# Performance work log

Hardware: AMD Instinct MI355X
Metric: run time of the kernel (lower is better)

The kernel has to match this reference:

```python
import jax, jax.numpy as jnp
import numpy as np

STRIDE = 4
EPS = 1e-6  # torch.pairwise_distance default eps


def setup_inputs() -> dict:
    key = jax.random.key(0)
    k1, k2 = jax.random.split(key)
    a = jax.random.normal(k1, (4, 256, 256, 256), dtype=jnp.float32)
    b = jax.random.normal(k2, (4, 256, 256, 256), dtype=jnp.float32)
    return {"a": a, "b": b}


def _patches(x, stride):
    # nn.Unfold(1, stride): sample every stride-th pixel -> [B, N, C]
    B, C, H, W = x.shape
    xp = x[:, :, ::stride, ::stride]            # [B, C, h, w]
    h, w = xp.shape[2], xp.shape[3]
    return xp.reshape(B, C, h * w).transpose(0, 2, 1), h, w


def reference(a, b):
    B, C, H, W = a.shape
    av, h, w = _patches(a, STRIDE)              # [B, N, C]
    bv, _, _ = _patches(b, STRIDE)              # [B, M, C]
    a2 = jnp.sum(av * av, axis=-1)              # [B, N]
    b2 = jnp.sum(bv * bv, axis=-1)              # [B, M]
    ab = jnp.einsum('bnc,bmc->bnm', av, bv)     # [B, N, M]
    sa = jnp.sum(av, axis=-1)
    sb = jnp.sum(bv, axis=-1)
    d2 = (a2[:, :, None] + b2[:, None, :] - 2.0 * ab
          + 2.0 * EPS * (sa[:, :, None] - sb[:, None, :]) + C * EPS * EPS)
    d2min = jnp.min(d2, axis=-1)                # sqrt is monotone -> min of d2 first
    l2 = jnp.sqrt(jnp.maximum(d2min, 0.0))      # [B, N]
    scores = 2.0 * jax.nn.sigmoid(-l2)
    sm = scores.reshape(B, h, w)
    # F.interpolate(..., mode='nearest') with integer scale == pixel repeat
    out = jnp.repeat(jnp.repeat(sm, STRIDE, axis=1), STRIDE, axis=2)
    return out[:, None, :, :]                   # [B, 1, H, W]
```

## Files before the change

kernel.cpp:

```cpp
#include <hip/hip_runtime.h>
#include <math.h>


#define BATCH 4
#define CH    256
#define HH    256
#define WW    256
#define NPTS  4096
#define EPSV  1e-6f

typedef _Float16 half8  __attribute__((ext_vector_type(8)));
typedef float    f32x4  __attribute__((ext_vector_type(4)));

typedef __attribute__((address_space(1))) const void global_cvoid;
typedef __attribute__((address_space(3))) void lds_void;

#define AC_OFF   0u
#define BC_OFF   (8u << 20)
#define A2_OFF   (16u << 20)
#define B2_OFF   ((16u << 20) + (64u << 10))
#define DP_OFF   ((16u << 20) + (128u << 10))
#define WS_TOTAL ((16u << 20) + (384u << 10))

__global__ __launch_bounds__(256) void gm_gather(
    const float* __restrict__ srcA, const float* __restrict__ srcB,
    unsigned char* __restrict__ ws)
{
  const int t  = threadIdx.x;
  const int h  = blockIdx.x;
  const int b  = blockIdx.y;
  const int z  = blockIdx.z;
  const int w  = t & 63;
  const int wv = t >> 6;

  const float* src = z ? srcB : srcA;
  unsigned char* dst = ws + (z ? BC_OFF : AC_OFF);
  float* norms = (float*)(ws + (z ? B2_OFF : A2_OFF));
  const float epsSign = z ? -2.0f * EPSV : 2.0f * EPSV;
  const float addC    = z ? (float)CH * EPSV * EPSV : 0.0f;

  const float* rowbase = src + ((size_t)b * CH) * (HH * WW)
                             + (size_t)(h * 4) * WW + (size_t)(w * 4);
  float ssum = 0.0f, ssq = 0.0f;
  #pragma unroll
  for (int i = 0; i < 8; ++i) {
    const int kc = wv * 8 + i;
    half8 hv;
    #pragma unroll
    for (int j = 0; j < 8; ++j) {
      const int c = kc * 8 + j;
      float v = rowbase[(size_t)c * (HH * WW)];
      ssum += v;
      ssq  = fmaf(v, v, ssq);
      hv[j] = (_Float16)v;
    }
    *reinterpret_cast<half8*>(dst + ((size_t)((b * 32 + kc) * NPTS + h * 64 + w)) * 16) = hv;
  }

  __shared__ float red[2][4][64];
  red[0][wv][w] = ssum;
  red[1][wv][w] = ssq;
  __syncthreads();
  if (t < 64) {
    float sm = red[0][0][t] + red[0][1][t] + red[0][2][t] + red[0][3][t];
    float sq = red[1][0][t] + red[1][1][t] + red[1][2][t] + red[1][3][t];
    norms[b * NPTS + h * 64 + t] = fmaf(epsSign, sm, sq) + addC;
  }
}

__device__ __forceinline__ void stage_b_tile(const unsigned char* __restrict__ Bc,
                                             int b, int mbase,
                                             unsigned char* dst, int t) {
  const int wv = t >> 6;
  #pragma unroll
  for (int r = 0; r < 8; ++r) {
    unsigned x  = (unsigned)(r * 256 + t) * 16;
    unsigned lb = x ^ (((x >> 9) & 7) << 4);
    unsigned m_l = lb >> 9;
    unsigned kcb = (lb & 511) >> 4;
    const unsigned char* srcp =
        Bc + ((size_t)((b * 32 + kcb) * NPTS + mbase + m_l)) * 16;
    __builtin_amdgcn_global_load_lds((global_cvoid*)srcp,
                                     (lds_void*)(dst + (r * 4096 + wv * 1024)),
                                     16, 0, 0);
  }
}

__global__ __launch_bounds__(256, 2) void gm_gemm_min(
    const unsigned char* __restrict__ Ac, const unsigned char* __restrict__ Bc,
    const float* __restrict__ a2p, const float* __restrict__ b2pc,
    float* __restrict__ d2part)
{
  __shared__ __align__(16) unsigned char smem[65536];

  const int t  = threadIdx.x;
  const int l  = t & 63;
  const int wv = t >> 6;
  const int q  = (l >> 4) & 3;

  const int orig    = blockIdx.x;
  const int logical = (orig & 7) * 64 + (orig >> 3);
  const int ns = logical & 31;
  const int mq = (logical >> 5) & 3;
  const int b  = logical >> 7;
  const int nbase  = ns * 128;
  const int mstart = mq * 1024;

  #pragma unroll
  for (int r = 0; r < 16; ++r) {
    unsigned x  = (unsigned)(r * 256 + t) * 16;
    unsigned lb = x ^ (((x >> 9) & 7) << 4);
    unsigned n_l = lb >> 9;
    unsigned kcb = (lb & 511) >> 4;
    const unsigned char* srcp =
        Ac + ((size_t)((b * 32 + kcb) * NPTS + nbase + n_l)) * 16;
    __builtin_amdgcn_global_load_lds((global_cvoid*)srcp,
                                     (lds_void*)(smem + (r * 4096 + wv * 1024)),
                                     16, 0, 0);
  }
  asm volatile("s_waitcnt vmcnt(0)" ::: "memory");
  __builtin_amdgcn_s_barrier();

  half8 af[2][8];
  #pragma unroll
  for (int nf = 0; nf < 2; ++nf) {
    const unsigned rr = wv * 32 + nf * 16 + (l & 15);
    const unsigned sw = (rr & 7) << 4;
    #pragma unroll
    for (int kk = 0; kk < 8; ++kk)
      af[nf][kk] = *reinterpret_cast<const half8*>(
          smem + ((rr * 512 + q * 16 + kk * 64) ^ sw));
  }
  asm volatile("s_waitcnt lgkmcnt(0)" ::: "memory");
  __builtin_amdgcn_s_barrier();

  float rmin[2][4];
  #pragma unroll
  for (int nf = 0; nf < 2; ++nf)
    #pragma unroll
    for (int r = 0; r < 4; ++r) rmin[nf][r] = 3.0e38f;

  stage_b_tile(Bc, b, mstart, smem, t);
  for (int mt = 0; mt < 16; ++mt) {
    unsigned char* cb = (mt & 1) ? smem + 32768 : smem;
    unsigned char* nb = (mt & 1) ? smem : smem + 32768;
    if (mt < 15) {
      stage_b_tile(Bc, b, mstart + (mt + 1) * 64, nb, t);
      asm volatile("s_waitcnt vmcnt(8)" ::: "memory");
    } else {
      asm volatile("s_waitcnt vmcnt(0)" ::: "memory");
    }
    __builtin_amdgcn_s_barrier();

    f32x4 acc[2][4];
    #pragma unroll
    for (int nf = 0; nf < 2; ++nf)
      #pragma unroll
      for (int ms = 0; ms < 4; ++ms) acc[nf][ms] = (f32x4){0.f, 0.f, 0.f, 0.f};

    #pragma unroll
    for (int kk = 0; kk < 8; ++kk) {
      half8 bf[4];
      #pragma unroll
      for (int ms = 0; ms < 4; ++ms) {
        const unsigned rrB = ms * 16 + (l & 15);
        bf[ms] = *reinterpret_cast<const half8*>(
            cb + ((rrB * 512 + q * 16 + kk * 64) ^ ((rrB & 7) << 4)));
      }
      #pragma unroll
      for (int ms = 0; ms < 4; ++ms) {
        acc[0][ms] = __builtin_amdgcn_mfma_f32_16x16x32_f16(af[0][kk], bf[ms], acc[0][ms], 0, 0, 0);
        acc[1][ms] = __builtin_amdgcn_mfma_f32_16x16x32_f16(af[1][kk], bf[ms], acc[1][ms], 0, 0, 0);
      }
    }

    const int mbase = mstart + mt * 64;
    #pragma unroll
    for (int ms = 0; ms < 4; ++ms) {
      const float bp = b2pc[b * NPTS + mbase + ms * 16 + (l & 15)];
      #pragma unroll
      for (int r = 0; r < 4; ++r) {
        rmin[0][r] = fminf(rmin[0][r], fmaf(-2.0f, acc[0][ms][r], bp));
        rmin[1][r] = fminf(rmin[1][r], fmaf(-2.0f, acc[1][ms][r], bp));
      }
    }
    __builtin_amdgcn_s_barrier();
  }

  #pragma unroll
  for (int nf = 0; nf < 2; ++nf)
    #pragma unroll
    for (int r = 0; r < 4; ++r) {
      float v = rmin[nf][r];
      v = fminf(v, __shfl_xor(v, 1, 64));
      v = fminf(v, __shfl_xor(v, 2, 64));
      v = fminf(v, __shfl_xor(v, 4, 64));
      v = fminf(v, __shfl_xor(v, 8, 64));
      if ((l & 15) == 0) {
        const int n = nbase + wv * 32 + nf * 16 + q * 4 + r;
        d2part[(size_t)(b * NPTS + n) * 4 + mq] = v + a2p[b * NPTS + n];
      }
    }
}

__global__ __launch_bounds__(256) void gm_finalize(
    const float* __restrict__ d2part, float* __restrict__ out)
{
  const int id = blockIdx.x * 256 + threadIdx.x;
  const f32x4 u = *reinterpret_cast<const f32x4*>(d2part + (size_t)id * 4);
  const float d2 = fminf(fminf(u[0], u[1]), fminf(u[2], u[3]));
  const float l2 = sqrtf(fmaxf(d2, 0.0f));
  const float s  = 2.0f / (1.0f + expf(l2));
  const int b = id >> 12;
  const int n = id & 4095;
  const int h = n >> 6, w = n & 63;
  float4 v = make_float4(s, s, s, s);
  float* obase = out + ((size_t)(b * 256 + h * 4)) * 256 + w * 4;
  #pragma unroll
  for (int i = 0; i < 4; ++i)
    *reinterpret_cast<float4*>(obase + (size_t)i * 256) = v;
}

__global__ void gm_sentinel(float* out) { out[0] = 1.0e6f; }

extern "C" void kernel_launch(void* const* d_in, const int* in_sizes, int n_in,
                              void* d_out, int out_size, void* d_ws, size_t ws_size,
                              hipStream_t stream) {
  const float* a = (const float*)d_in[0];
  const float* b = (const float*)d_in[1];
  float* out = (float*)d_out;
  unsigned char* ws = (unsigned char*)d_ws;

  if (ws_size < (size_t)WS_TOTAL) {
    gm_sentinel<<<1, 1, 0, stream>>>(out);
    return;
  }

  gm_gather<<<dim3(64, 4, 2), 256, 0, stream>>>(a, b, ws);
  gm_gemm_min<<<512, 256, 0, stream>>>(
      ws + AC_OFF, ws + BC_OFF,
      (const float*)(ws + A2_OFF), (const float*)(ws + B2_OFF),
      (float*)(ws + DP_OFF));
  gm_finalize<<<64, 256, 0, stream>>>((const float*)(ws + DP_OFF), out);
}
```

Baseline: 75.18 us.

## Double block size, deepen B-tile pipeline to four LDS stages, cache b2 in LDS

The GEMM-min kernel now runs 512-thread blocks, each covering 256 query points, so every staged B tile is shared by twice as many rows and the grid halves to 256 blocks. The B pipeline becomes a 4-slot ring prefetched three tiles ahead, which drops the trailing barrier per iteration, and the b2 norms are preloaded into LDS instead of read from global memory each iteration. MFMA sections get raised wave priority. The cost is 128KB+ of LDS per block, which may allow only one block per CU, and 256 blocks may underfill the GPU.

```diff
diff --git a/kernel.cpp b/kernel.cpp
--- a/kernel.cpp
+++ b/kernel.cpp
@@ -73,25 +73,26 @@
                                              unsigned char* dst, int t) {
   const int wv = t >> 6;
   #pragma unroll
-  for (int r = 0; r < 8; ++r) {
-    unsigned x  = (unsigned)(r * 256 + t) * 16;
+  for (int r = 0; r < 4; ++r) {
+    unsigned x  = (unsigned)(r * 512 + t) * 16;
     unsigned lb = x ^ (((x >> 9) & 7) << 4);
     unsigned m_l = lb >> 9;
     unsigned kcb = (lb & 511) >> 4;
     const unsigned char* srcp =
         Bc + ((size_t)((b * 32 + kcb) * NPTS + mbase + m_l)) * 16;
     __builtin_amdgcn_global_load_lds((global_cvoid*)srcp,
-                                     (lds_void*)(dst + (r * 4096 + wv * 1024)),
+                                     (lds_void*)(dst + (r * 8192 + wv * 1024)),
                                      16, 0, 0);
   }
 }
 
-__global__ __launch_bounds__(256, 2) void gm_gemm_min(
+__global__ __launch_bounds__(512, 2) void gm_gemm_min(
     const unsigned char* __restrict__ Ac, const unsigned char* __restrict__ Bc,
     const float* __restrict__ a2p, const float* __restrict__ b2pc,
     float* __restrict__ d2part)
 {
-  __shared__ __align__(16) unsigned char smem[65536];
+  __shared__ __align__(16) unsigned char smem[131072];
+  __shared__ float sB2[1024];
 
   const int t  = threadIdx.x;
   const int l  = t & 63;
@@ -99,26 +100,29 @@
   const int q  = (l >> 4) & 3;
 
   const int orig    = blockIdx.x;
-  const int logical = (orig & 7) * 64 + (orig >> 3);
-  const int ns = logical & 31;
-  const int mq = (logical >> 5) & 3;
-  const int b  = logical >> 7;
-  const int nbase  = ns * 128;
+  const int logical = (orig & 7) * 32 + (orig >> 3);
+  const int ns = logical & 15;
+  const int mq = (logical >> 4) & 3;
+  const int b  = logical >> 6;
+  const int nbase  = ns * 256;
   const int mstart = mq * 1024;
 
   #pragma unroll
   for (int r = 0; r < 16; ++r) {
-    unsigned x  = (unsigned)(r * 256 + t) * 16;
+    unsigned x  = (unsigned)(r * 512 + t) * 16;
     unsigned lb = x ^ (((x >> 9) & 7) << 4);
     unsigned n_l = lb >> 9;
     unsigned kcb = (lb & 511) >> 4;
     const unsigned char* srcp =
         Ac + ((size_t)((b * 32 + kcb) * NPTS + nbase + n_l)) * 16;
     __builtin_amdgcn_global_load_lds((global_cvoid*)srcp,
-                                     (lds_void*)(smem + (r * 4096 + wv * 1024)),
+                                     (lds_void*)(smem + (r * 8192 + wv * 1024)),
                                      16, 0, 0);
   }
-  asm volatile("s_waitcnt vmcnt(0)" ::: "memory");
+  sB2[t]       = b2pc[b * NPTS + mstart + t];
+  sB2[t + 512] = b2pc[b * NPTS + mstart + t + 512];
+
+  asm volatile("s_waitcnt vmcnt(0) lgkmcnt(0)" ::: "memory");
   __builtin_amdgcn_s_barrier();
 
   half8 af[2][8];
@@ -140,24 +144,29 @@
     #pragma unroll
     for (int r = 0; r < 4; ++r) rmin[nf][r] = 3.0e38f;
 
-  stage_b_tile(Bc, b, mstart, smem, t);
+  stage_b_tile(Bc, b, mstart +   0, smem,          t);
+  stage_b_tile(Bc, b, mstart +  64, smem + 32768,  t);
+  stage_b_tile(Bc, b, mstart + 128, smem + 65536,  t);
+
   for (int mt = 0; mt < 16; ++mt) {
-    unsigned char* cb = (mt & 1) ? smem + 32768 : smem;
-    unsigned char* nb = (mt & 1) ? smem : smem + 32768;
-    if (mt < 15) {
-      stage_b_tile(Bc, b, mstart + (mt + 1) * 64, nb, t);
-      asm volatile("s_waitcnt vmcnt(8)" ::: "memory");
-    } else {
-      asm volatile("s_waitcnt vmcnt(0)" ::: "memory");
-    }
+    if (mt <= 13)      asm volatile("s_waitcnt vmcnt(8)" ::: "memory");
+    else if (mt == 14) asm volatile("s_waitcnt vmcnt(4)" ::: "memory");
+    else               asm volatile("s_waitcnt vmcnt(0)" ::: "memory");
     __builtin_amdgcn_s_barrier();
 
+    if (mt <= 12)
+      stage_b_tile(Bc, b, mstart + (mt + 3) * 64,
+                   smem + (unsigned)((mt + 3) & 3) * 32768, t);
+
+    const unsigned char* cb = smem + (unsigned)(mt & 3) * 32768;
+
     f32x4 acc[2][4];
     #pragma unroll
     for (int nf = 0; nf < 2; ++nf)
       #pragma unroll
       for (int ms = 0; ms < 4; ++ms) acc[nf][ms] = (f32x4){0.f, 0.f, 0.f, 0.f};
 
+    __builtin_amdgcn_s_setprio(1);
     #pragma unroll
     for (int kk = 0; kk < 8; ++kk) {
       half8 bf[4];
@@ -173,18 +182,17 @@
         acc[1][ms] = __builtin_amdgcn_mfma_f32_16x16x32_f16(af[1][kk], bf[ms], acc[1][ms], 0, 0, 0);
       }
     }
-
-    const int mbase = mstart + mt * 64;
+    __builtin_amdgcn_s_setprio(0);
+
     #pragma unroll
     for (int ms = 0; ms < 4; ++ms) {
-      const float bp = b2pc[b * NPTS + mbase + ms * 16 + (l & 15)];
+      const float bp = sB2[mt * 64 + ms * 16 + (l & 15)];
       #pragma unroll
       for (int r = 0; r < 4; ++r) {
         rmin[0][r] = fminf(rmin[0][r], fmaf(-2.0f, acc[0][ms][r], bp));
         rmin[1][r] = fminf(rmin[1][r], fmaf(-2.0f, acc[1][ms][r], bp));
       }
     }
-    __builtin_amdgcn_s_barrier();
   }
 
   #pragma unroll
@@ -237,7 +245,7 @@
   }
 
   gm_gather<<<dim3(64, 4, 2), 256, 0, stream>>>(a, b, ws);
-  gm_gemm_min<<<512, 256, 0, stream>>>(
+  gm_gemm_min<<<256, 512, 0, stream>>>(
       ws + AC_OFF, ws + BC_OFF,
       (const float*)(ws + A2_OFF), (const float*)(ws + B2_OFF),
       (float*)(ws + DP_OFF));
```

Result: faster. 72.71 us (-3.3%).

## Overlap batch 2-3 gather with batch 0-1 GEMM using 512-thread blocks

Applied to the files above, without the earlier changes.

Splits the work by batch: one kernel gathers batches 0-1, a second kernel runs the GEMM-min for batches 0-1 while other blocks gather batches 2-3, and a third runs the GEMM for batches 2-3. The aim is to hide the memory-bound gather behind MFMA compute. Blocks grow to 512 threads with larger N tiles (256) and fewer M subtiles, and the partial-min buffer widens to 8 slots. It also loads float4 in the gather but uses only the x lane, and raises wave priority around the MFMA loop.

```diff
diff --git a/kernel.cpp b/kernel.cpp
--- a/kernel.cpp
+++ b/kernel.cpp
@@ -6,6 +6,7 @@
 #define CH    256
 #define HH    256
 #define WW    256
+#define HW    (HH*WW)
 #define NPTS  4096
 #define EPSV  1e-6f
 
@@ -20,36 +21,32 @@
 #define A2_OFF   (16u << 20)
 #define B2_OFF   ((16u << 20) + (64u << 10))
 #define DP_OFF   ((16u << 20) + (128u << 10))
-#define WS_TOTAL ((16u << 20) + (384u << 10))
-
-__global__ __launch_bounds__(256) void gm_gather(
-    const float* __restrict__ srcA, const float* __restrict__ srcB,
-    unsigned char* __restrict__ ws)
-{
-  const int t  = threadIdx.x;
-  const int h  = blockIdx.x;
-  const int b  = blockIdx.y;
-  const int z  = blockIdx.z;
+#define WS_TOTAL ((16u << 20) + (640u << 10))
+
+__device__ __forceinline__ void gather_unit(const float* __restrict__ src,
+                                            unsigned char* __restrict__ ws,
+                                            int b, int h, int z, int t,
+                                            float* red )
+{
   const int w  = t & 63;
   const int wv = t >> 6;
-
-  const float* src = z ? srcB : srcA;
   unsigned char* dst = ws + (z ? BC_OFF : AC_OFF);
   float* norms = (float*)(ws + (z ? B2_OFF : A2_OFF));
   const float epsSign = z ? -2.0f * EPSV : 2.0f * EPSV;
   const float addC    = z ? (float)CH * EPSV * EPSV : 0.0f;
 
-  const float* rowbase = src + ((size_t)b * CH) * (HH * WW)
+  const float* rowbase = src + ((size_t)b * CH) * HW
                              + (size_t)(h * 4) * WW + (size_t)(w * 4);
   float ssum = 0.0f, ssq = 0.0f;
   #pragma unroll
-  for (int i = 0; i < 8; ++i) {
-    const int kc = wv * 8 + i;
+  for (int i = 0; i < 4; ++i) {
+    const int kc = wv * 4 + i;
     half8 hv;
     #pragma unroll
     for (int j = 0; j < 8; ++j) {
       const int c = kc * 8 + j;
-      float v = rowbase[(size_t)c * (HH * WW)];
+      const float4 v4 = *reinterpret_cast<const float4*>(rowbase + (size_t)c * HW);
+      const float v = v4.x;
       ssum += v;
       ssq  = fmaf(v, v, ssq);
       hv[j] = (_Float16)v;
@@ -57,13 +54,16 @@
     *reinterpret_cast<half8*>(dst + ((size_t)((b * 32 + kc) * NPTS + h * 64 + w)) * 16) = hv;
   }
 
-  __shared__ float red[2][4][64];
-  red[0][wv][w] = ssum;
-  red[1][wv][w] = ssq;
+  red[(0 * 8 + wv) * 64 + w] = ssum;
+  red[(1 * 8 + wv) * 64 + w] = ssq;
   __syncthreads();
   if (t < 64) {
-    float sm = red[0][0][t] + red[0][1][t] + red[0][2][t] + red[0][3][t];
-    float sq = red[1][0][t] + red[1][1][t] + red[1][2][t] + red[1][3][t];
+    float sm = 0.f, sq = 0.f;
+    #pragma unroll
+    for (int g = 0; g < 8; ++g) {
+      sm += red[(0 * 8 + g) * 64 + t];
+      sq += red[(1 * 8 + g) * 64 + t];
+    }
     norms[b * NPTS + h * 64 + t] = fmaf(epsSign, sm, sq) + addC;
   }
 }
@@ -73,66 +73,63 @@
                                              unsigned char* dst, int t) {
   const int wv = t >> 6;
   #pragma unroll
-  for (int r = 0; r < 8; ++r) {
-    unsigned x  = (unsigned)(r * 256 + t) * 16;
+  for (int r = 0; r < 4; ++r) {
+    unsigned x  = (unsigned)(r * 512 + t) * 16;
     unsigned lb = x ^ (((x >> 9) & 7) << 4);
     unsigned m_l = lb >> 9;
     unsigned kcb = (lb & 511) >> 4;
     const unsigned char* srcp =
         Bc + ((size_t)((b * 32 + kcb) * NPTS + mbase + m_l)) * 16;
     __builtin_amdgcn_global_load_lds((global_cvoid*)srcp,
-                                     (lds_void*)(dst + (r * 4096 + wv * 1024)),
+                                     (lds_void*)(dst + (r * 8192 + wv * 1024)),
                                      16, 0, 0);
   }
 }
 
-__global__ __launch_bounds__(256, 2) void gm_gemm_min(
-    const unsigned char* __restrict__ Ac, const unsigned char* __restrict__ Bc,
-    const float* __restrict__ a2p, const float* __restrict__ b2pc,
-    float* __restrict__ d2part)
-{
-  __shared__ __align__(16) unsigned char smem[65536];
-
-  const int t  = threadIdx.x;
+template<int NSUB>
+__device__ __forceinline__ void gemm_tile(const unsigned char* __restrict__ Ac,
+                                          const unsigned char* __restrict__ Bc,
+                                          const float* __restrict__ a2p,
+                                          const float* __restrict__ b2pc,
+                                          float* __restrict__ d2part,
+                                          int b, int nbase, int mstart, int slot,
+                                          int t, unsigned char* smem)
+{
   const int l  = t & 63;
   const int wv = t >> 6;
   const int q  = (l >> 4) & 3;
 
-  const int orig    = blockIdx.x;
-  const int logical = (orig & 7) * 64 + (orig >> 3);
-  const int ns = logical & 31;
-  const int mq = (logical >> 5) & 3;
-  const int b  = logical >> 7;
-  const int nbase  = ns * 128;
-  const int mstart = mq * 1024;
-
-  #pragma unroll
-  for (int r = 0; r < 16; ++r) {
-    unsigned x  = (unsigned)(r * 256 + t) * 16;
-    unsigned lb = x ^ (((x >> 9) & 7) << 4);
-    unsigned n_l = lb >> 9;
-    unsigned kcb = (lb & 511) >> 4;
-    const unsigned char* srcp =
-        Ac + ((size_t)((b * 32 + kcb) * NPTS + nbase + n_l)) * 16;
-    __builtin_amdgcn_global_load_lds((global_cvoid*)srcp,
-                                     (lds_void*)(smem + (r * 4096 + wv * 1024)),
-                                     16, 0, 0);
-  }
-  asm volatile("s_waitcnt vmcnt(0)" ::: "memory");
-  __builtin_amdgcn_s_barrier();
-
   half8 af[2][8];
   #pragma unroll
-  for (int nf = 0; nf < 2; ++nf) {
-    const unsigned rr = wv * 32 + nf * 16 + (l & 15);
-    const unsigned sw = (rr & 7) << 4;
-    #pragma unroll
-    for (int kk = 0; kk < 8; ++kk)
-      af[nf][kk] = *reinterpret_cast<const half8*>(
-          smem + ((rr * 512 + q * 16 + kk * 64) ^ sw));
-  }
-  asm volatile("s_waitcnt lgkmcnt(0)" ::: "memory");
-  __builtin_amdgcn_s_barrier();
+  for (int hf = 0; hf < 2; ++hf) {
+    #pragma unroll
+    for (int r = 0; r < 8; ++r) {
+      unsigned x  = (unsigned)(r * 512 + t) * 16;
+      unsigned lb = x ^ (((x >> 9) & 7) << 4);
+      unsigned n_l = lb >> 9;
+      unsigned kcb = (lb & 511) >> 4;
+      const unsigned char* srcp =
+          Ac + ((size_t)((b * 32 + kcb) * NPTS + nbase + hf * 128 + n_l)) * 16;
+      __builtin_amdgcn_global_load_lds((global_cvoid*)srcp,
+                                       (lds_void*)(smem + (r * 8192 + wv * 1024)),
+                                       16, 0, 0);
+    }
+    asm volatile("s_waitcnt vmcnt(0)" ::: "memory");
+    __builtin_amdgcn_s_barrier();
+    if ((wv >> 2) == hf) {
+      #pragma unroll
+      for (int nf = 0; nf < 2; ++nf) {
+        const unsigned rr = (wv & 3) * 32 + nf * 16 + (l & 15);
+        const unsigned sw = (rr & 7) << 4;
+        #pragma unroll
+        for (int kk = 0; kk < 8; ++kk)
+          af[nf][kk] = *reinterpret_cast<const half8*>(
+              smem + ((rr * 512 + q * 16 + kk * 64) ^ sw));
+      }
+    }
+    asm volatile("s_waitcnt lgkmcnt(0)" ::: "memory");
+    __builtin_amdgcn_s_barrier();
+  }
 
   float rmin[2][4];
   #pragma unroll
@@ -141,12 +138,12 @@
     for (int r = 0; r < 4; ++r) rmin[nf][r] = 3.0e38f;
 
   stage_b_tile(Bc, b, mstart, smem, t);
-  for (int mt = 0; mt < 16; ++mt) {
+  for (int mt = 0; mt < NSUB; ++mt) {
     unsigned char* cb = (mt & 1) ? smem + 32768 : smem;
     unsigned char* nb = (mt & 1) ? smem : smem + 32768;
-    if (mt < 15) {
+    if (mt < NSUB - 1) {
       stage_b_tile(Bc, b, mstart + (mt + 1) * 64, nb, t);
-      asm volatile("s_waitcnt vmcnt(8)" ::: "memory");
+      asm volatile("s_waitcnt vmcnt(4)" ::: "memory");
     } else {
       asm volatile("s_waitcnt vmcnt(0)" ::: "memory");
     }
@@ -158,6 +155,7 @@
       #pragma unroll
       for (int ms = 0; ms < 4; ++ms) acc[nf][ms] = (f32x4){0.f, 0.f, 0.f, 0.f};
 
+    __builtin_amdgcn_s_setprio(1);
     #pragma unroll
     for (int kk = 0; kk < 8; ++kk) {
       half8 bf[4];
@@ -173,6 +171,7 @@
         acc[1][ms] = __builtin_amdgcn_mfma_f32_16x16x32_f16(af[1][kk], bf[ms], acc[1][ms], 0, 0, 0);
       }
     }
+    __builtin_amdgcn_s_setprio(0);
 
     const int mbase = mstart + mt * 64;
     #pragma unroll
@@ -198,17 +197,64 @@
       v = fminf(v, __shfl_xor(v, 8, 64));
       if ((l & 15) == 0) {
         const int n = nbase + wv * 32 + nf * 16 + q * 4 + r;
-        d2part[(size_t)(b * NPTS + n) * 4 + mq] = v + a2p[b * NPTS + n];
-      }
-    }
+        d2part[(size_t)(b * NPTS + n) * 8 + slot] = v + a2p[b * NPTS + n];
+      }
+    }
+}
+
+__global__ __launch_bounds__(512) void gm_k1_gather01(
+    const float* __restrict__ A, const float* __restrict__ B,
+    unsigned char* __restrict__ ws)
+{
+  __shared__ float red[1024];
+  const int bid = blockIdx.x;
+  const int h = bid & 63, z = (bid >> 6) & 1, b = bid >> 7;
+  gather_unit(z ? B : A, ws, b, h, z, threadIdx.x, red);
+}
+
+__global__ __launch_bounds__(512, 2) void gm_k2_gemm01_gather23(
+    const float* __restrict__ A, const float* __restrict__ B,
+    unsigned char* __restrict__ ws)
+{
+  __shared__ __align__(16) unsigned char smem[65536];
+  const int bid = blockIdx.x;
+  const int t   = threadIdx.x;
+  const int idx = ((bid >> 4) << 3) | (bid & 7);
+  if (bid & 8) {
+    const int h = idx & 63, z = (idx >> 6) & 1, b = 2 + (idx >> 7);
+    gather_unit(z ? B : A, ws, b, h, z, t, (float*)smem);
+  } else {
+    const int ns = (idx & 7) | (((idx >> 3) & 1) << 3);
+    const int mh = (idx >> 4) & 7;
+    const int b  = idx >> 7;
+    gemm_tile<8>(ws + AC_OFF, ws + BC_OFF,
+                 (const float*)(ws + A2_OFF), (const float*)(ws + B2_OFF),
+                 (float*)(ws + DP_OFF), b, ns * 256, mh * 512, mh, t, smem);
+  }
+}
+
+__global__ __launch_bounds__(512, 2) void gm_k3_gemm23(
+    unsigned char* __restrict__ ws)
+{
+  __shared__ __align__(16) unsigned char smem[65536];
+  const int bid = blockIdx.x;
+  const int ns = (bid & 7) | (((bid >> 3) & 1) << 3);
+  const int mh = (bid >> 4) & 7;
+  const int b  = 2 + (bid >> 7);
+  gemm_tile<8>(ws + AC_OFF, ws + BC_OFF,
+               (const float*)(ws + A2_OFF), (const float*)(ws + B2_OFF),
+               (float*)(ws + DP_OFF), b, ns * 256, mh * 512, mh,
+               threadIdx.x, smem);
 }
 
 __global__ __launch_bounds__(256) void gm_finalize(
     const float* __restrict__ d2part, float* __restrict__ out)
 {
   const int id = blockIdx.x * 256 + threadIdx.x;
-  const f32x4 u = *reinterpret_cast<const f32x4*>(d2part + (size_t)id * 4);
-  const float d2 = fminf(fminf(u[0], u[1]), fminf(u[2], u[3]));
+  const f32x4 u  = *reinterpret_cast<const f32x4*>(d2part + (size_t)id * 8);
+  const f32x4 w4 = *reinterpret_cast<const f32x4*>(d2part + (size_t)id * 8 + 4);
+  const float d2 = fminf(fminf(fminf(u[0], u[1]), fminf(u[2], u[3])),
+                         fminf(fminf(w4[0], w4[1]), fminf(w4[2], w4[3])));
   const float l2 = sqrtf(fmaxf(d2, 0.0f));
   const float s  = 2.0f / (1.0f + expf(l2));
   const int b = id >> 12;
@@ -236,10 +282,8 @@
     return;
   }
 
-  gm_gather<<<dim3(64, 4, 2), 256, 0, stream>>>(a, b, ws);
-  gm_gemm_min<<<512, 256, 0, stream>>>(
-      ws + AC_OFF, ws + BC_OFF,
-      (const float*)(ws + A2_OFF), (const float*)(ws + B2_OFF),
-      (float*)(ws + DP_OFF));
+  gm_k1_gather01<<<256, 512, 0, stream>>>(a, b, ws);
+  gm_k2_gemm01_gather23<<<512, 512, 0, stream>>>(a, b, ws);
+  gm_k3_gemm23<<<256, 512, 0, stream>>>(ws);
   gm_finalize<<<64, 256, 0, stream>>>((const float*)(ws + DP_OFF), out);
 }
```

New measurement: 84.37 us. +12.2%, slower.
